# Optimization experiments

Measured on AMD Instinct MI355X. Metric: run time of the kernel, lower is better.

The kernel has to match this reference:

```python
import jax, jax.numpy as jnp
import numpy as np

N = 16384          # number of units
K = 655
BOOST_STRENGTH = 1.0


def setup_inputs() -> dict:
    key = jax.random.key(0)
    k1, k2 = jax.random.split(key)
    x = jax.random.normal(k1, (4096, N), dtype=jnp.float32)
    dutyCycle = jax.random.uniform(k2, (N,), dtype=jnp.float32)
    return {"x": x, "dutyCycle": dutyCycle}


def reference(x, dutyCycle):
    # boost factor per unit: encourages under-used units
    targetDensity = K / x.shape[1]
    boostFactors = jnp.exp((targetDensity - dutyCycle) * BOOST_STRENGTH)  # (N,)
    boosted = x * boostFactors  # (B, N)
    # top-k per row, then scatter a binary mask of winners
    _, idx = jax.lax.top_k(boosted, K)  # (B, K)
    b = jnp.arange(x.shape[0])[:, None]  # (B, 1)
    res = jnp.zeros_like(x).at[b, idx].set(1.0)
    return res
```

## Files before the change

### kernel.cpp

```cpp
#include <hip/hip_runtime.h>
#include <math.h>
#include <stdint.h>


#define N_UNITS 16384
#define K_WIN 655
#define NT 512
#define NPROBE 11
#define CAP 2048

__device__ __forceinline__ uint32_t fkey(float f) {
    uint32_t b = __float_as_uint(f);
    uint32_t m = (uint32_t)((int32_t)b >> 31) | 0x80000000u;
    return b ^ m;
}

__global__ void boost_kernel(const float* __restrict__ duty,
                             float* __restrict__ bf, int n) {
    int i = blockIdx.x * blockDim.x + threadIdx.x;
    if (i < n) {
        const float td = 0.03997802734375f;
        float s = td - duty[i];
        bf[i] = (float)exp((double)s);
    }
}

__global__ __launch_bounds__(NT, 6) void kwinners_kernel(
    const float* __restrict__ x, const float* __restrict__ bf,
    float* __restrict__ out) {
    __shared__ __align__(16) uint32_t khiw[N_UNITS / 2];
    __shared__ uint32_t red[(NT / 64) * NPROBE];
    __shared__ int cglob[NPROBE];
    __shared__ uint32_t cand_idx[CAP];
    __shared__ uint32_t cand_key[CAP];
    __shared__ int prb[NPROBE];
    __shared__ int sc[2];

    const int tid = threadIdx.x;
    const int lane = tid & 63;
    const int w = tid >> 6;
    const int row = blockIdx.x;
    const float4* xrow = (const float4*)(x + (size_t)row * N_UNITS);
    const float4* bfv = (const float4*)bf;
    float* orow = out + (size_t)row * N_UNITS;

    if (tid < NPROBE) {
        const float pv[NPROBE] = {1.90f, 1.70f, 1.55f, 1.43f, 1.33f, 1.25f,
                                  1.18f, 1.12f, 1.06f, 0.99f, 0.90f};
        prb[tid] = (int)(fkey(pv[tid]) >> 16);
    }
    if (tid == 0) sc[0] = 0;
    __syncthreads();

    int P[NPROBE];
#pragma unroll
    for (int p = 0; p < NPROBE; ++p) P[p] = prb[p];
    int cnt[NPROBE];
#pragma unroll
    for (int p = 0; p < NPROBE; ++p) cnt[p] = 0;

#pragma unroll
    for (int j = 0; j < N_UNITS / (NT * 4); ++j) {
        int i4 = tid + j * NT;
        float4 xv = xrow[i4];
        float4 bv = bfv[i4];
        int h0 = (int)(fkey(xv.x * bv.x) >> 16);
        int h1 = (int)(fkey(xv.y * bv.y) >> 16);
        int h2 = (int)(fkey(xv.z * bv.z) >> 16);
        int h3 = (int)(fkey(xv.w * bv.w) >> 16);
        uint2 pk;
        pk.x = (uint32_t)h0 | ((uint32_t)h1 << 16);
        pk.y = (uint32_t)h2 | ((uint32_t)h3 << 16);
        ((uint2*)khiw)[i4] = pk;
#pragma unroll
        for (int p = 0; p < NPROBE; ++p)
            cnt[p] += (h0 > P[p]) + (h1 > P[p]) + (h2 > P[p]) + (h3 > P[p]);
    }

    auto reduce_counts = [&]() {
#pragma unroll
        for (int p = 0; p < NPROBE; ++p) {
            int v = cnt[p];
#pragma unroll
            for (int m = 32; m >= 1; m >>= 1) v += __shfl_xor(v, m, 64);
            if (lane == 0) red[w * NPROBE + p] = (uint32_t)v;
        }
        __syncthreads();
        if (tid < NPROBE) {
            int s = 0;
#pragma unroll
            for (int ww = 0; ww < NT / 64; ++ww) s += (int)red[ww * NPROBE + tid];
            cglob[tid] = s;
        }
        __syncthreads();
    };
    reduce_counts();

    int lo, hi, cab, cgl;
    {
        int j = 0;
        while (j < NPROBE && cglob[j] < K_WIN) ++j;
        if (j == 0) {
            lo = P[0]; cgl = cglob[0]; hi = 65535; cab = 0;
        } else if (j == NPROBE) {
            lo = -1; cgl = N_UNITS; hi = P[NPROBE - 1]; cab = cglob[NPROBE - 1];
        } else {
            lo = P[j]; cgl = cglob[j]; hi = P[j - 1]; cab = cglob[j - 1];
        }
    }
    int m = cgl - cab;

    while (m > CAP && (hi - lo) > 1) {
        __syncthreads();
        if (tid < NPROBE)
            prb[tid] = lo + (int)(((long)(hi - lo) * (NPROBE - tid)) / (NPROBE + 1));
        __syncthreads();
#pragma unroll
        for (int p = 0; p < NPROBE; ++p) P[p] = prb[p];
#pragma unroll
        for (int p = 0; p < NPROBE; ++p) cnt[p] = 0;
        for (int j = 0; j < 4; ++j) {
            uint4 wv = ((const uint4*)khiw)[tid + j * NT];
            int h0 = (int)(wv.x & 0xFFFFu), h1 = (int)(wv.x >> 16);
            int h2 = (int)(wv.y & 0xFFFFu), h3 = (int)(wv.y >> 16);
            int h4 = (int)(wv.z & 0xFFFFu), h5 = (int)(wv.z >> 16);
            int h6 = (int)(wv.w & 0xFFFFu), h7 = (int)(wv.w >> 16);
#pragma unroll
            for (int p = 0; p < NPROBE; ++p)
                cnt[p] += (h0 > P[p]) + (h1 > P[p]) + (h2 > P[p]) + (h3 > P[p]) +
                          (h4 > P[p]) + (h5 > P[p]) + (h6 > P[p]) + (h7 > P[p]);
        }
        reduce_counts();
        int j = 0;
        while (j < NPROBE && cglob[j] < K_WIN) ++j;
        if (j == 0) {
            lo = P[0]; cgl = cglob[0];
        } else if (j == NPROBE) {
            hi = P[NPROBE - 1]; cab = cglob[NPROBE - 1];
        } else {
            lo = P[j]; cgl = cglob[j]; hi = P[j - 1]; cab = cglob[j - 1];
        }
        m = cgl - cab;
    }

    for (int j = 0; j < 4; ++j) {
        int q = tid + j * NT;
        uint4 wv = ((const uint4*)khiw)[q];
        int base = q * 8;
        int h[8] = {(int)(wv.x & 0xFFFFu), (int)(wv.x >> 16),
                    (int)(wv.y & 0xFFFFu), (int)(wv.y >> 16),
                    (int)(wv.z & 0xFFFFu), (int)(wv.z >> 16),
                    (int)(wv.w & 0xFFFFu), (int)(wv.w >> 16)};
#pragma unroll
        for (int e = 0; e < 8; ++e) {
            if (h[e] > lo && h[e] <= hi) {
                int p = atomicAdd(&sc[0], 1);
                if (p < CAP) cand_idx[p] = (uint32_t)(base + e);
            }
        }
    }
    __syncthreads();
    const int mm = sc[0];
    const int need = K_WIN - cab;

    const float* xr = x + (size_t)row * N_UNITS;
    const int mc = (mm <= CAP) ? mm : 0;
    for (int j = tid; j < mc; j += NT) {
        int i = (int)cand_idx[j];
        cand_key[j] = fkey(xr[i] * bf[i]);
    }

    for (int j = 0; j < N_UNITS / (NT * 4); ++j) {
        int f = tid + j * NT;
        uint2 wv = ((const uint2*)khiw)[f];
        float4 o;
        o.x = ((int)(wv.x & 0xFFFFu) > hi) ? 1.0f : 0.0f;
        o.y = ((int)(wv.x >> 16) > hi) ? 1.0f : 0.0f;
        o.z = ((int)(wv.y & 0xFFFFu) > hi) ? 1.0f : 0.0f;
        o.w = ((int)(wv.y >> 16) > hi) ? 1.0f : 0.0f;
        ((float4*)orow)[f] = o;
    }
    __syncthreads();

    if (mm <= CAP) {
        for (int j = tid; j < mm; j += NT) {
            uint32_t myk = cand_key[j];
            uint32_t myi = cand_idx[j];
            int r = 0;
            for (int l = 0; l < mm; ++l) {
                uint32_t lk = cand_key[l];
                r += (lk > myk) || (lk == myk && cand_idx[l] < myi);
            }
            if (r < need) orow[myi] = 1.0f;
        }
    } else if (tid == 0) {
        uint32_t* h8 = cand_idx;
        for (int b = 0; b < 256; ++b) h8[b] = 0;
        for (int i = 0; i < N_UNITS; ++i) {
            int h = (int)((khiw[i >> 1] >> ((i & 1) * 16)) & 0xFFFFu);
            if (h == hi) h8[(fkey(xr[i] * bf[i]) & 0xFFFFu) >> 8]++;
        }
        int acc = 0, d1 = 0, need2 = 0;
        for (int b = 255; b >= 0; --b) {
            int c = (int)h8[b];
            if (acc + c >= need) { d1 = b; need2 = need - acc; break; }
            acc += c;
        }
        for (int b = 0; b < 256; ++b) h8[b] = 0;
        for (int i = 0; i < N_UNITS; ++i) {
            int h = (int)((khiw[i >> 1] >> ((i & 1) * 16)) & 0xFFFFu);
            if (h == hi) {
                uint32_t kl = fkey(xr[i] * bf[i]) & 0xFFFFu;
                if ((int)(kl >> 8) == d1) h8[kl & 0xFFu]++;
            }
        }
        int acc2 = 0, d2 = 0, need3 = 0;
        for (int b = 255; b >= 0; --b) {
            int c = (int)h8[b];
            if (acc2 + c >= need2) { d2 = b; need3 = need2 - acc2; break; }
            acc2 += c;
        }
        uint32_t Tlo = ((uint32_t)d1 << 8) | (uint32_t)d2;
        int r = 0;
        for (int i = 0; i < N_UNITS; ++i) {
            int h = (int)((khiw[i >> 1] >> ((i & 1) * 16)) & 0xFFFFu);
            if (h == hi) {
                uint32_t kl = fkey(xr[i] * bf[i]) & 0xFFFFu;
                if (kl > Tlo) orow[i] = 1.0f;
                else if (kl == Tlo && r < need3) { orow[i] = 1.0f; ++r; }
            }
        }
    }
}

extern "C" void kernel_launch(void* const* d_in, const int* in_sizes, int n_in,
                              void* d_out, int out_size, void* d_ws,
                              size_t ws_size, hipStream_t stream) {
    const float* x = (const float*)d_in[0];
    const float* duty = (const float*)d_in[1];
    float* out = (float*)d_out;
    float* bf = (float*)d_ws;

    hipLaunchKernelGGL(boost_kernel, dim3(N_UNITS / 256), dim3(256), 0, stream,
                       duty, bf, N_UNITS);
    int rows = out_size / N_UNITS;
    hipLaunchKernelGGL(kwinners_kernel, dim3(rows), dim3(NT), 0, stream, x, bf,
                       out);
}
```

Before: 451.4 us.

## Tighten probe set, fuse candidate collection with mask write, use nontemporal IO

Cuts the initial probe thresholds from 11 to 5 hardcoded 16-bit key values and shrinks the candidate cap from 2048 to 512, which lowers register and LDS use so the launch bound can rise to 8 blocks per CU. The candidate-gather pass is merged with the output mask write so the key array in shared memory is scanned once. Input loads and output stores become nontemporal to avoid polluting cache with streaming data. The risk is more refinement iterations or falling back to the serial single-thread path when more than 512 candidates land in the bracket.

```diff
diff --git a/kernel.cpp b/kernel.cpp
--- a/kernel.cpp
+++ b/kernel.cpp
@@ -6,8 +6,10 @@
 #define N_UNITS 16384
 #define K_WIN 655
 #define NT 512
-#define NPROBE 11
-#define CAP 2048
+#define NPROBE 5
+#define CAP 512
+
+typedef float f32x4 __attribute__((ext_vector_type(4)));
 
 __device__ __forceinline__ uint32_t fkey(float f) {
     uint32_t b = __float_as_uint(f);
@@ -25,7 +27,7 @@
     }
 }
 
-__global__ __launch_bounds__(NT, 6) void kwinners_kernel(
+__global__ __launch_bounds__(NT, 8) void kwinners_kernel(
     const float* __restrict__ x, const float* __restrict__ bf,
     float* __restrict__ out) {
     __shared__ __align__(16) uint32_t khiw[N_UNITS / 2];
@@ -40,21 +42,14 @@
     const int lane = tid & 63;
     const int w = tid >> 6;
     const int row = blockIdx.x;
-    const float4* xrow = (const float4*)(x + (size_t)row * N_UNITS);
-    const float4* bfv = (const float4*)bf;
+    const f32x4* xrow = (const f32x4*)(x + (size_t)row * N_UNITS);
+    const f32x4* bfv = (const f32x4*)bf;
     float* orow = out + (size_t)row * N_UNITS;
 
-    if (tid < NPROBE) {
-        const float pv[NPROBE] = {1.90f, 1.70f, 1.55f, 1.43f, 1.33f, 1.25f,
-                                  1.18f, 1.12f, 1.06f, 0.99f, 0.90f};
-        prb[tid] = (int)(fkey(pv[tid]) >> 16);
-    }
     if (tid == 0) sc[0] = 0;
     __syncthreads();
 
-    int P[NPROBE];
-#pragma unroll
-    for (int p = 0; p < NPROBE; ++p) P[p] = prb[p];
+    int P[NPROBE] = {0xBFC0, 0xBFA6, 0xBF9A, 0xBF8F, 0xBF66};
     int cnt[NPROBE];
 #pragma unroll
     for (int p = 0; p < NPROBE; ++p) cnt[p] = 0;
@@ -62,8 +57,8 @@
 #pragma unroll
     for (int j = 0; j < N_UNITS / (NT * 4); ++j) {
         int i4 = tid + j * NT;
-        float4 xv = xrow[i4];
-        float4 bv = bfv[i4];
+        f32x4 xv = __builtin_nontemporal_load(xrow + i4);
+        f32x4 bv = bfv[i4];
         int h0 = (int)(fkey(xv.x * bv.x) >> 16);
         int h1 = (int)(fkey(xv.y * bv.y) >> 16);
         int h2 = (int)(fkey(xv.z * bv.z) >> 16);
@@ -143,20 +138,33 @@
         m = cgl - cab;
     }
 
-    for (int j = 0; j < 4; ++j) {
+    for (int j = 0; j < N_UNITS / (NT * 4); ++j) {
         int q = tid + j * NT;
-        uint4 wv = ((const uint4*)khiw)[q];
-        int base = q * 8;
-        int h[8] = {(int)(wv.x & 0xFFFFu), (int)(wv.x >> 16),
-                    (int)(wv.y & 0xFFFFu), (int)(wv.y >> 16),
-                    (int)(wv.z & 0xFFFFu), (int)(wv.z >> 16),
-                    (int)(wv.w & 0xFFFFu), (int)(wv.w >> 16)};
-#pragma unroll
-        for (int e = 0; e < 8; ++e) {
-            if (h[e] > lo && h[e] <= hi) {
-                int p = atomicAdd(&sc[0], 1);
-                if (p < CAP) cand_idx[p] = (uint32_t)(base + e);
-            }
+        uint2 wv = ((const uint2*)khiw)[q];
+        int h0 = (int)(wv.x & 0xFFFFu), h1 = (int)(wv.x >> 16);
+        int h2 = (int)(wv.y & 0xFFFFu), h3 = (int)(wv.y >> 16);
+        f32x4 o;
+        o.x = (h0 > hi) ? 1.0f : 0.0f;
+        o.y = (h1 > hi) ? 1.0f : 0.0f;
+        o.z = (h2 > hi) ? 1.0f : 0.0f;
+        o.w = (h3 > hi) ? 1.0f : 0.0f;
+        __builtin_nontemporal_store(o, ((f32x4*)orow) + q);
+        int base = q * 4;
+        if (h0 > lo && h0 <= hi) {
+            int p = atomicAdd(&sc[0], 1);
+            if (p < CAP) cand_idx[p] = (uint32_t)(base + 0);
+        }
+        if (h1 > lo && h1 <= hi) {
+            int p = atomicAdd(&sc[0], 1);
+            if (p < CAP) cand_idx[p] = (uint32_t)(base + 1);
+        }
+        if (h2 > lo && h2 <= hi) {
+            int p = atomicAdd(&sc[0], 1);
+            if (p < CAP) cand_idx[p] = (uint32_t)(base + 2);
+        }
+        if (h3 > lo && h3 <= hi) {
+            int p = atomicAdd(&sc[0], 1);
+            if (p < CAP) cand_idx[p] = (uint32_t)(base + 3);
         }
     }
     __syncthreads();
@@ -168,17 +176,6 @@
     for (int j = tid; j < mc; j += NT) {
         int i = (int)cand_idx[j];
         cand_key[j] = fkey(xr[i] * bf[i]);
-    }
-
-    for (int j = 0; j < N_UNITS / (NT * 4); ++j) {
-        int f = tid + j * NT;
-        uint2 wv = ((const uint2*)khiw)[f];
-        float4 o;
-        o.x = ((int)(wv.x & 0xFFFFu) > hi) ? 1.0f : 0.0f;
-        o.y = ((int)(wv.x >> 16) > hi) ? 1.0f : 0.0f;
-        o.z = ((int)(wv.y & 0xFFFFu) > hi) ? 1.0f : 0.0f;
-        o.w = ((int)(wv.y >> 16) > hi) ? 1.0f : 0.0f;
-        ((float4*)orow)[f] = o;
     }
     __syncthreads();
 
```

Measured after the change: 547.3 us. +21.2%, slower.
